# Kernel tuning notes

Hardware: AMD Instinct MI355X
Metric: run time of the kernel (lower is better)

Reference implementation:

```python
import jax, jax.numpy as jnp
import numpy as np

B, D, C = 256, 512, 100000
U_M, L_M = 0.8, 0.45
U_A, L_A = 110.0, 10.0
LAMBDA_G = 35.0
SCALE = 64.0


def setup_inputs() -> dict:
    key = jax.random.key(0)
    k1, k2, k3, k4 = jax.random.split(key, 4)
    x = jax.random.normal(k1, (B, D), dtype=jnp.float32)
    # per-sample feature magnitudes in [l_a, u_a]
    x_norm = L_A + jax.random.uniform(k2, (B, 1), dtype=jnp.float32) * (U_A - L_A)
    labels = jax.random.randint(k3, (B,), 0, C)
    weight = jax.random.normal(k4, (C, D), dtype=jnp.float32)
    return {"x": x, "x_norm": x_norm, "labels": labels, "weight": weight}


def reference(x, x_norm, labels, weight):
    # adaptive margin m(a) = slope * (a - l_a) + l_m, per sample [B,1]
    ada_margin = (U_M - L_M) / (U_A - L_A) * (x_norm - L_A) + L_M
    cos_m = jnp.cos(ada_margin)
    sin_m = jnp.sin(ada_margin)

    xn = x / jnp.linalg.norm(x, axis=-1, keepdims=True)          # [B,D]
    wn = weight / jnp.linalg.norm(weight, axis=-1, keepdims=True)  # [C,D]
    cos_theta = jnp.clip(jnp.einsum('bd,cd->bc', xn, wn), -1.0, 1.0)  # [B,C]
    sin_theta = jnp.sqrt(1.0 - cos_theta * cos_theta)
    cos_theta_m = cos_theta * cos_m - sin_theta * sin_m
    # easy_margin=True: only apply margin where cos_theta > 0
    cos_theta_m = jnp.where(cos_theta > 0, cos_theta_m, cos_theta)

    one_hot = jax.nn.one_hot(labels, C, dtype=cos_theta.dtype)   # [B,C]
    logits = SCALE * (one_hot * cos_theta_m + (1.0 - one_hot) * cos_theta)

    # cross-entropy with mean reduction
    tgt = jnp.take_along_axis(logits, labels[:, None], axis=1)[:, 0]
    ce = jnp.mean(jax.nn.logsumexp(logits, axis=1) - tgt)

    # MagFace G-loss: mean(a / u_a^2 + 1/a)
    loss_g = jnp.mean(x_norm / (U_A * U_A) + 1.0 / x_norm)
    return ce + LAMBDA_G * loss_g
```

## Files before the change

### kernel.cpp

```cpp
#include <hip/hip_runtime.h>
#include <hip/hip_bf16.h>

#define BB 256
#define DD 512
#define CNUM 100000
#define CPAD 100096
#define NCHUNK 782
#define NPART (NCHUNK * 2)

typedef __attribute__((ext_vector_type(8))) short bf16x8;
typedef __attribute__((ext_vector_type(4))) float f32x4;

typedef __attribute__((address_space(1))) void gvoid_t;
typedef __attribute__((address_space(3))) void lvoid_t;

__device__ __forceinline__ void gload16(const void* g, void* l) {
  __builtin_amdgcn_global_load_lds((const gvoid_t*)g, (lvoid_t*)l, 16, 0, 0);
}

__device__ __forceinline__ unsigned short f2bf(float f) {
  union { float f; unsigned int u; } v; v.f = f;
  unsigned int u = v.u;
  unsigned int r = u + 0x7FFFu + ((u >> 16) & 1u);
  return (unsigned short)(r >> 16);
}

__global__ void k_prep_x(const float* __restrict__ x, const float* __restrict__ xnrm,
                         unsigned short* __restrict__ xn, float* __restrict__ cm,
                         float* __restrict__ sm) {
  int b = blockIdx.x;
  int lane = threadIdx.x;
  const float4* xr = (const float4*)(x + (size_t)b * DD);
  float4 v0 = xr[lane * 2];
  float4 v1 = xr[lane * 2 + 1];
  float ss = v0.x * v0.x + v0.y * v0.y + v0.z * v0.z + v0.w * v0.w +
             v1.x * v1.x + v1.y * v1.y + v1.z * v1.z + v1.w * v1.w;
#pragma unroll
  for (int msk = 1; msk < 64; msk <<= 1) ss += __shfl_xor(ss, msk, 64);
  float inv = rsqrtf(ss);
  unsigned int p0 = (unsigned int)f2bf(v0.x * inv) | ((unsigned int)f2bf(v0.y * inv) << 16);
  unsigned int p1 = (unsigned int)f2bf(v0.z * inv) | ((unsigned int)f2bf(v0.w * inv) << 16);
  unsigned int p2 = (unsigned int)f2bf(v1.x * inv) | ((unsigned int)f2bf(v1.y * inv) << 16);
  unsigned int p3 = (unsigned int)f2bf(v1.z * inv) | ((unsigned int)f2bf(v1.w * inv) << 16);
  *(uint4*)(xn + (size_t)b * DD + lane * 8) = make_uint4(p0, p1, p2, p3);
  if (lane == 0) {
    float a = xnrm[b];
    float marg = 0.0035f * (a - 10.0f) + 0.45f;
    cm[b] = cosf(marg);
    sm[b] = sinf(marg);
  }
}

__global__ __launch_bounds__(512) void k_gemm(
    const unsigned short* __restrict__ xn, const float* __restrict__ w,
    const int* __restrict__ labels, const float* __restrict__ cmv,
    const float* __restrict__ smv, float2* __restrict__ part, float* __restrict__ tgt) {
  __shared__ short Xs[BB * 64];
  __shared__ short Ws[128 * 64];
  __shared__ float sInvW[128];
  __shared__ int sLab[BB];
  __shared__ float sCm[BB], sSm[BB];

  int tid = threadIdx.x, wave = tid >> 6, lane = tid & 63;
  int wm = wave >> 1, wq = wave & 1;
  int cbase = blockIdx.x * 128;

  if (tid < BB) {
    sLab[tid] = labels[tid];
    sCm[tid] = cmv[tid];
    sSm[tid] = smv[tid];
  }

  f32x4 acc[4][4];
#pragma unroll
  for (int m = 0; m < 4; ++m)
#pragma unroll
    for (int n = 0; n < 4; ++n) acc[m][n] = (f32x4){0.f, 0.f, 0.f, 0.f};

  int lr = lane >> 3;
  int lk = (lane & 7) ^ lr;

  int wrow = tid >> 2, wseg = tid & 3;
  bool wvalid = (cbase + wrow) < CNUM;
  const float* wptr = w + (size_t)(cbase + wrow) * DD + wseg * 16;
  float ssacc = 0.0f;
  int wsw0 = wrow * 64 + ((wseg * 16) ^ ((wrow & 7) << 3));
  int wsw1 = wrow * 64 + ((wseg * 16 + 8) ^ ((wrow & 7) << 3));

  for (int kc = 0; kc < 8; ++kc) {
    int k0 = kc * 64;
    float4 a0, a1, a2, a3;
    if (wvalid) {
      const float4* wp = (const float4*)(wptr + k0);
      a0 = wp[0]; a1 = wp[1]; a2 = wp[2]; a3 = wp[3];
    } else {
      a0 = a1 = a2 = a3 = make_float4(0.f, 0.f, 0.f, 0.f);
    }
    __syncthreads();
#pragma unroll
    for (int i = 0; i < 4; ++i) {
      int rbase = i * 64 + wave * 8;
      gload16(xn + (size_t)(rbase + lr) * DD + k0 + lk * 8, &Xs[rbase * 64]);
    }
    ssacc += a0.x * a0.x + a0.y * a0.y + a0.z * a0.z + a0.w * a0.w +
             a1.x * a1.x + a1.y * a1.y + a1.z * a1.z + a1.w * a1.w +
             a2.x * a2.x + a2.y * a2.y + a2.z * a2.z + a2.w * a2.w +
             a3.x * a3.x + a3.y * a3.y + a3.z * a3.z + a3.w * a3.w;
    unsigned int q0 = (unsigned int)f2bf(a0.x) | ((unsigned int)f2bf(a0.y) << 16);
    unsigned int q1 = (unsigned int)f2bf(a0.z) | ((unsigned int)f2bf(a0.w) << 16);
    unsigned int q2 = (unsigned int)f2bf(a1.x) | ((unsigned int)f2bf(a1.y) << 16);
    unsigned int q3 = (unsigned int)f2bf(a1.z) | ((unsigned int)f2bf(a1.w) << 16);
    unsigned int q4 = (unsigned int)f2bf(a2.x) | ((unsigned int)f2bf(a2.y) << 16);
    unsigned int q5 = (unsigned int)f2bf(a2.z) | ((unsigned int)f2bf(a2.w) << 16);
    unsigned int q6 = (unsigned int)f2bf(a3.x) | ((unsigned int)f2bf(a3.y) << 16);
    unsigned int q7 = (unsigned int)f2bf(a3.z) | ((unsigned int)f2bf(a3.w) << 16);
    *(uint4*)&Ws[wsw0] = make_uint4(q0, q1, q2, q3);
    *(uint4*)&Ws[wsw1] = make_uint4(q4, q5, q6, q7);
    __syncthreads();
#pragma unroll
    for (int ks = 0; ks < 2; ++ks) {
      int krd = ks * 32 + (lane >> 4) * 8;
      int swz = (lane & 7) << 3;
      bf16x8 af[4], bfr[4];
#pragma unroll
      for (int m = 0; m < 4; ++m) {
        int ra = wm * 64 + m * 16 + (lane & 15);
        af[m] = *(const bf16x8*)&Xs[ra * 64 + (krd ^ swz)];
      }
#pragma unroll
      for (int n = 0; n < 4; ++n) {
        int rb = wq * 64 + n * 16 + (lane & 15);
        bfr[n] = *(const bf16x8*)&Ws[rb * 64 + (krd ^ swz)];
      }
#pragma unroll
      for (int m = 0; m < 4; ++m)
#pragma unroll
        for (int n = 0; n < 4; ++n)
          acc[m][n] = __builtin_amdgcn_mfma_f32_16x16x32_bf16(af[m], bfr[n], acc[m][n], 0, 0, 0);
    }
  }

  ssacc += __shfl_xor(ssacc, 1, 64);
  ssacc += __shfl_xor(ssacc, 2, 64);
  if (wseg == 0) sInvW[wrow] = wvalid ? rsqrtf(ssacc) : 0.0f;
  __syncthreads();

  int g = lane >> 4, cb = lane & 15;
  float invc[4];
#pragma unroll
  for (int n = 0; n < 4; ++n) invc[n] = sInvW[wq * 64 + n * 16 + cb];
#pragma unroll
  for (int m = 0; m < 4; ++m) {
#pragma unroll
    for (int r = 0; r < 4; ++r) {
      int row = wm * 64 + m * 16 + g * 4 + r;
      int lab = sLab[row];
      float cmr = sCm[row], smr = sSm[row];
      float lg[4];
      float vmax = -1e30f;
#pragma unroll
      for (int n = 0; n < 4; ++n) {
        int col = cbase + wq * 64 + n * 16 + cb;
        float cv = acc[m][n][r] * invc[n];
        cv = fminf(1.0f, fmaxf(-1.0f, cv));
        float logit;
        if (col == lab) {
          float st = sqrtf(fmaxf(0.0f, 1.0f - cv * cv));
          float cm2 = cv * cmr - st * smr;
          logit = 64.0f * (cv > 0.0f ? cm2 : cv);
          tgt[row] = logit;
        } else {
          logit = 64.0f * cv;
        }
        if (col >= CNUM) logit = -1e30f;
        lg[n] = logit;
        vmax = fmaxf(vmax, logit);
      }
#pragma unroll
      for (int msk = 1; msk < 16; msk <<= 1) vmax = fmaxf(vmax, __shfl_xor(vmax, msk, 64));
      float s = 0.0f;
#pragma unroll
      for (int n = 0; n < 4; ++n) s += __expf(lg[n] - vmax);
#pragma unroll
      for (int msk = 1; msk < 16; msk <<= 1) s += __shfl_xor(s, msk, 64);
      if (cb == 0) part[(size_t)row * NPART + blockIdx.x * 2 + wq] = make_float2(vmax, s);
    }
  }
}

__global__ void k_merge(const float2* __restrict__ part, const float* __restrict__ tgt,
                        float* __restrict__ ce) {
  int b = blockIdx.x, t = threadIdx.x;
  float m = -1e30f, s = 0.0f;
  for (int i = t; i < NPART; i += 256) {
    float2 p = part[(size_t)b * NPART + i];
    float nm = fmaxf(m, p.x);
    s = s * __expf(m - nm) + p.y * __expf(p.x - nm);
    m = nm;
  }
  __shared__ float smx[256], ssm[256];
  smx[t] = m;
  ssm[t] = s;
  __syncthreads();
  for (int off = 128; off > 0; off >>= 1) {
    if (t < off) {
      float m2 = smx[t + off], s2 = ssm[t + off];
      float nm = fmaxf(smx[t], m2);
      ssm[t] = ssm[t] * __expf(smx[t] - nm) + s2 * __expf(m2 - nm);
      smx[t] = nm;
    }
    __syncthreads();
  }
  if (t == 0) ce[b] = smx[0] + logf(ssm[0]) - tgt[b];
}

__global__ void k_final(const float* __restrict__ ce, const float* __restrict__ xnrm,
                        float* __restrict__ out) {
  int t = threadIdx.x;
  float cv = ce[t];
  float a = xnrm[t];
  float gv = a * (1.0f / (110.0f * 110.0f)) + 1.0f / a;
  __shared__ float s1[256], s2[256];
  s1[t] = cv;
  s2[t] = gv;
  __syncthreads();
  for (int off = 128; off > 0; off >>= 1) {
    if (t < off) {
      s1[t] += s1[t + off];
      s2[t] += s2[t + off];
    }
    __syncthreads();
  }
  if (t == 0) out[0] = s1[0] * (1.0f / 256.0f) + 35.0f * s2[0] * (1.0f / 256.0f);
}

extern "C" void kernel_launch(void* const* d_in, const int* in_sizes, int n_in,
                              void* d_out, int out_size, void* d_ws, size_t ws_size,
                              hipStream_t stream) {
  const float* x = (const float*)d_in[0];
  const float* xnrm = (const float*)d_in[1];
  const int* labels = (const int*)d_in[2];
  const float* w = (const float*)d_in[3];

  char* ws = (char*)d_ws;
  unsigned short* XN = (unsigned short*)ws;
  size_t off = (size_t)BB * DD * 2;
  float* CM = (float*)(ws + off);  off += 1024;
  float* SM = (float*)(ws + off);  off += 1024;
  float* TGT = (float*)(ws + off); off += 1024;
  float* CE = (float*)(ws + off);  off += 1024;
  float2* PART = (float2*)(ws + off);

  k_prep_x<<<BB, 64, 0, stream>>>(x, xnrm, XN, CM, SM);
  k_gemm<<<NCHUNK, 512, 0, stream>>>(XN, w, labels, CM, SM, PART, TGT);
  k_merge<<<BB, 256, 0, stream>>>(PART, TGT, CE);
  k_final<<<1, 256, 0, stream>>>(CE, xnrm, (float*)d_out);
}
```

Measured before the change: 83.21 us.

## Prefetch next weight chunk into registers with manual waitcnt barriers

Double-buffers the fp32 weight loads in registers so the next k-chunk's global loads are issued before the MFMA compute of the current chunk, using explicit s_waitcnt/s_barrier instead of __syncthreads. Out-of-range weight rows are clamped to a valid row and masked at the epilogue instead of branching. Also adds a launch bound hint of 4 blocks per CU. Risks register pressure/spills and relies on the compiler's load ordering matching the vmcnt counts.

```diff
diff --git a/kernel.cpp b/kernel.cpp
--- a/kernel.cpp
+++ b/kernel.cpp
@@ -51,7 +51,7 @@
   }
 }
 
-__global__ __launch_bounds__(512) void k_gemm(
+__global__ __launch_bounds__(512, 4) void k_gemm(
     const unsigned short* __restrict__ xn, const float* __restrict__ w,
     const int* __restrict__ labels, const float* __restrict__ cmv,
     const float* __restrict__ smv, float2* __restrict__ part, float* __restrict__ tgt) {
@@ -70,53 +70,64 @@
     sCm[tid] = cmv[tid];
     sSm[tid] = smv[tid];
   }
-
-  f32x4 acc[4][4];
-#pragma unroll
-  for (int m = 0; m < 4; ++m)
-#pragma unroll
-    for (int n = 0; n < 4; ++n) acc[m][n] = (f32x4){0.f, 0.f, 0.f, 0.f};
+  __syncthreads();
 
   int lr = lane >> 3;
   int lk = (lane & 7) ^ lr;
 
   int wrow = tid >> 2, wseg = tid & 3;
-  bool wvalid = (cbase + wrow) < CNUM;
-  const float* wptr = w + (size_t)(cbase + wrow) * DD + wseg * 16;
+  int wr_clamped = cbase + wrow;
+  if (wr_clamped >= CNUM) wr_clamped = 0;
+  const float* wptr = w + (size_t)wr_clamped * DD + wseg * 16;
   float ssacc = 0.0f;
   int wsw0 = wrow * 64 + ((wseg * 16) ^ ((wrow & 7) << 3));
   int wsw1 = wrow * 64 + ((wseg * 16 + 8) ^ ((wrow & 7) << 3));
 
+  f32x4 acc[4][4];
+#pragma unroll
+  for (int m = 0; m < 4; ++m)
+#pragma unroll
+    for (int n = 0; n < 4; ++n) acc[m][n] = (f32x4){0.f, 0.f, 0.f, 0.f};
+
+  f32x4 wv[4];
+#pragma unroll
+  for (int j = 0; j < 4; ++j) wv[j] = *(const f32x4*)(wptr + j * 4);
+
+#pragma unroll
   for (int kc = 0; kc < 8; ++kc) {
-    int k0 = kc * 64;
-    float4 a0, a1, a2, a3;
-    if (wvalid) {
-      const float4* wp = (const float4*)(wptr + k0);
-      a0 = wp[0]; a1 = wp[1]; a2 = wp[2]; a3 = wp[3];
-    } else {
-      a0 = a1 = a2 = a3 = make_float4(0.f, 0.f, 0.f, 0.f);
-    }
-    __syncthreads();
+    const int k0 = kc * 64;
+    asm volatile("s_barrier" ::: "memory");
 #pragma unroll
     for (int i = 0; i < 4; ++i) {
       int rbase = i * 64 + wave * 8;
       gload16(xn + (size_t)(rbase + lr) * DD + k0 + lk * 8, &Xs[rbase * 64]);
     }
-    ssacc += a0.x * a0.x + a0.y * a0.y + a0.z * a0.z + a0.w * a0.w +
-             a1.x * a1.x + a1.y * a1.y + a1.z * a1.z + a1.w * a1.w +
-             a2.x * a2.x + a2.y * a2.y + a2.z * a2.z + a2.w * a2.w +
-             a3.x * a3.x + a3.y * a3.y + a3.z * a3.z + a3.w * a3.w;
-    unsigned int q0 = (unsigned int)f2bf(a0.x) | ((unsigned int)f2bf(a0.y) << 16);
-    unsigned int q1 = (unsigned int)f2bf(a0.z) | ((unsigned int)f2bf(a0.w) << 16);
-    unsigned int q2 = (unsigned int)f2bf(a1.x) | ((unsigned int)f2bf(a1.y) << 16);
-    unsigned int q3 = (unsigned int)f2bf(a1.z) | ((unsigned int)f2bf(a1.w) << 16);
-    unsigned int q4 = (unsigned int)f2bf(a2.x) | ((unsigned int)f2bf(a2.y) << 16);
-    unsigned int q5 = (unsigned int)f2bf(a2.z) | ((unsigned int)f2bf(a2.w) << 16);
-    unsigned int q6 = (unsigned int)f2bf(a3.x) | ((unsigned int)f2bf(a3.y) << 16);
-    unsigned int q7 = (unsigned int)f2bf(a3.z) | ((unsigned int)f2bf(a3.w) << 16);
-    *(uint4*)&Ws[wsw0] = make_uint4(q0, q1, q2, q3);
-    *(uint4*)&Ws[wsw1] = make_uint4(q4, q5, q6, q7);
-    __syncthreads();
+    asm volatile("s_waitcnt vmcnt(4)" ::: "memory");
+    {
+      f32x4 a = wv[0], b = wv[1], c = wv[2], d = wv[3];
+      ssacc += a[0]*a[0] + a[1]*a[1] + a[2]*a[2] + a[3]*a[3] +
+               b[0]*b[0] + b[1]*b[1] + b[2]*b[2] + b[3]*b[3] +
+               c[0]*c[0] + c[1]*c[1] + c[2]*c[2] + c[3]*c[3] +
+               d[0]*d[0] + d[1]*d[1] + d[2]*d[2] + d[3]*d[3];
+      unsigned int q0 = (unsigned int)f2bf(a[0]) | ((unsigned int)f2bf(a[1]) << 16);
+      unsigned int q1 = (unsigned int)f2bf(a[2]) | ((unsigned int)f2bf(a[3]) << 16);
+      unsigned int q2 = (unsigned int)f2bf(b[0]) | ((unsigned int)f2bf(b[1]) << 16);
+      unsigned int q3 = (unsigned int)f2bf(b[2]) | ((unsigned int)f2bf(b[3]) << 16);
+      unsigned int q4 = (unsigned int)f2bf(c[0]) | ((unsigned int)f2bf(c[1]) << 16);
+      unsigned int q5 = (unsigned int)f2bf(c[2]) | ((unsigned int)f2bf(c[3]) << 16);
+      unsigned int q6 = (unsigned int)f2bf(d[0]) | ((unsigned int)f2bf(d[1]) << 16);
+      unsigned int q7 = (unsigned int)f2bf(d[2]) | ((unsigned int)f2bf(d[3]) << 16);
+      *(uint4*)&Ws[wsw0] = make_uint4(q0, q1, q2, q3);
+      *(uint4*)&Ws[wsw1] = make_uint4(q4, q5, q6, q7);
+    }
+    if (kc < 7) {
+#pragma unroll
+      for (int j = 0; j < 4; ++j) wv[j] = *(const f32x4*)(wptr + (kc + 1) * 64 + j * 4);
+      asm volatile("s_waitcnt vmcnt(4) lgkmcnt(0)" ::: "memory");
+    } else {
+      asm volatile("s_waitcnt vmcnt(0) lgkmcnt(0)" ::: "memory");
+    }
+    asm volatile("s_barrier" ::: "memory");
 #pragma unroll
     for (int ks = 0; ks < 2; ++ks) {
       int krd = ks * 32 + (lane >> 4) * 8;
@@ -142,13 +153,16 @@
 
   ssacc += __shfl_xor(ssacc, 1, 64);
   ssacc += __shfl_xor(ssacc, 2, 64);
-  if (wseg == 0) sInvW[wrow] = wvalid ? rsqrtf(ssacc) : 0.0f;
+  if (wseg == 0) sInvW[wrow] = rsqrtf(ssacc);
   __syncthreads();
 
   int g = lane >> 4, cb = lane & 15;
   float invc[4];
 #pragma unroll
-  for (int n = 0; n < 4; ++n) invc[n] = sInvW[wq * 64 + n * 16 + cb];
+  for (int n = 0; n < 4; ++n) {
+    int col = cbase + wq * 64 + n * 16 + cb;
+    invc[n] = (col < CNUM) ? sInvW[wq * 64 + n * 16 + cb] : 0.0f;
+  }
 #pragma unroll
   for (int m = 0; m < 4; ++m) {
 #pragma unroll
```

New measurement: 102.1 us. 22.7% more time.
